# Optimization experiments

Measured on AMD Instinct MI355X. Metric: run time of the kernel, lower is better.

## Reference

```python
import jax, jax.numpy as jnp
import numpy as np

B, N, D_IMG, D_TXT, H, C = 256, 100, 1024, 768, 512, 512
NBLK = 8
EPS = 1e-5


def setup_inputs() -> dict:
    key = jax.random.key(0)
    ks = jax.random.split(key, 24)
    rn = lambda k, s, sc=0.04: jax.random.normal(k, s, jnp.float32) * sc
    return {
        "img_embedding": jax.random.normal(ks[0], (B, D_IMG), jnp.float32),
        "func_text_embedding": jax.random.normal(ks[1], (B, D_TXT), jnp.float32),
        "node_emb": jax.random.normal(ks[2], (B, N, 768), jnp.float32),
        "pos_emb": jax.random.uniform(ks[3], (B, N, 4), jnp.float32),
        # swin head
        "swinbn_g": jnp.ones((D_IMG,)), "swinbn_b": jnp.zeros((D_IMG,)),
        "swinfc_w": rn(ks[4], (H, D_IMG)), "swinfc_b": jnp.zeros((H,)),
        # text head
        "bntext_g": jnp.ones((D_TXT,)), "bntext_b": jnp.zeros((D_TXT,)),
        "fctext_w": rn(ks[5], (H, D_TXT)), "fctext_b": jnp.zeros((H,)),
        # node / bbox heads (BatchNorm1d over channel dim = max_node)
        "bngat_g": jnp.ones((N,)), "bngat_b": jnp.zeros((N,)),
        "fcgat_w": rn(ks[6], (480, 768)), "fcgat_b": jnp.zeros((480,)),
        "bnbbox_g": jnp.ones((N,)), "bnbbox_b": jnp.zeros((N,)),
        "fcbbox_w": rn(ks[7], (32, 4), 0.3), "fcbbox_b": jnp.zeros((32,)),
        # 8 stacked Rs_GCN non-local blocks (1x1 conv weights = [out,in])
        "gcn_theta_w": rn(ks[8], (NBLK, C, C)), "gcn_theta_b": jnp.zeros((NBLK, C)),
        "gcn_phi_w": rn(ks[9], (NBLK, C, C)), "gcn_phi_b": jnp.zeros((NBLK, C)),
        "gcn_g_w": rn(ks[10], (NBLK, C, C)), "gcn_g_b": jnp.zeros((NBLK, C)),
        "gcn_W_w": rn(ks[11], (NBLK, C, C)), "gcn_W_b": jnp.zeros((NBLK, C)),
        "gcn_bn_g": jnp.ones((NBLK, C)), "gcn_bn_b": jnp.zeros((NBLK, C)),
        # final classifier
        "ffbn_g": jnp.ones((3 * H,)), "ffbn_b": jnp.zeros((3 * H,)),
        "ff_w": rn(ks[12], (2, 3 * H)), "ff_b": jnp.zeros((2,)),
    }


def _bn2(x, g, b):  # BatchNorm1d on (B, C), training-mode batch stats
    m = x.mean(0)
    v = x.var(0)
    return (x - m) * jax.lax.rsqrt(v + EPS) * g + b


def _bn_ch(x, g, b):  # BatchNorm1d on (B, C, L), channel axis 1
    m = x.mean((0, 2), keepdims=True)
    v = x.var((0, 2), keepdims=True)
    return (x - m) * jax.lax.rsqrt(v + EPS) * g[None, :, None] + b[None, :, None]


def reference(img_embedding, func_text_embedding, node_emb, pos_emb,
              swinbn_g, swinbn_b, swinfc_w, swinfc_b,
              bntext_g, bntext_b, fctext_w, fctext_b,
              bngat_g, bngat_b, fcgat_w, fcgat_b,
              bnbbox_g, bnbbox_b, fcbbox_w, fcbbox_b,
              gcn_theta_w, gcn_theta_b, gcn_phi_w, gcn_phi_b,
              gcn_g_w, gcn_g_b, gcn_W_w, gcn_W_b, gcn_bn_g, gcn_bn_b,
              ffbn_g, ffbn_b, ff_w, ff_b):
    elu = jax.nn.elu
    # image branch: x = elu(swinfc(swinbn(img)))
    x = elu(_bn2(img_embedding, swinbn_g, swinbn_b) @ swinfc_w.T + swinfc_b)
    # text branch: elu(fc_text(bn_text(text)))
    ft = elu(_bn2(func_text_embedding, bntext_g, bntext_b) @ fctext_w.T + fctext_b)
    # node / bbox branches (BN over node dim, then linear over feature dim)
    h = elu(_bn_ch(node_emb, bngat_g, bngat_b) @ fcgat_w.T + fcgat_b)       # (B,N,480)
    p = elu(_bn_ch(pos_emb, bnbbox_g, bnbbox_b) @ fcbbox_w.T + fcbbox_b)    # (B,N,32)
    v = jnp.concatenate([h, p], axis=2).transpose(0, 2, 1)                  # (B,512,N)

    # 8 non-local Rs_GCN blocks
    for i in range(NBLK):
        g_v = jnp.einsum('oc,bcn->bno', gcn_g_w[i], v) + gcn_g_b[i]          # (B,N,C)
        th_v = jnp.einsum('oc,bcn->bno', gcn_theta_w[i], v) + gcn_theta_b[i]  # (B,N,C)
        ph_v = jnp.einsum('oc,bcn->bon', gcn_phi_w[i], v) + gcn_phi_b[i][:, None]  # (B,C,N)
        R = jnp.einsum('bnc,bcm->bnm', th_v, ph_v)                            # (B,N,N)
        A = jax.nn.softmax(R, axis=-1)
        y = jnp.einsum('bnm,bmc->bcn', A, g_v)                                # (B,C,N)
        Wy = jnp.einsum('oc,bcn->bon', gcn_W_w[i], y) + gcn_W_b[i][:, None]
        Wy = _bn_ch(Wy, gcn_bn_g[i], gcn_bn_b[i])
        v = Wy + v                                                            # residual

    emb = v.transpose(0, 2, 1)  # (B,N,512)
    # l2norm normalizes over dim=1 (the node dim), matching the torch code
    emb = emb / jnp.sqrt(jnp.sum(emb * emb, axis=1, keepdims=True))
    h_feature = emb.mean(axis=1)  # (B,512)

    all_feats = jnp.concatenate([x, h_feature, ft], axis=1)  # (B,1536)
    out = _bn2(all_feats, ffbn_g, ffbn_b) @ ff_w.T + ff_b    # (B,2)
    return out
```

## Files before the change

### kernel.cpp

```cpp
#include <hip/hip_runtime.h>
#include <cstddef>

#define EPS 1e-5f

constexpr int Bsz = 256;
constexpr int Nn  = 100;
constexpr int Cc  = 512;
constexpr int BN_ROWS = Bsz * Nn;

__device__ __forceinline__ void gload_lds16(const void* g, void* l) {
    __builtin_amdgcn_global_load_lds(
        (const __attribute__((address_space(1))) void*)g,
        (__attribute__((address_space(3))) void*)l, 16, 0, 0);
}

__global__ void colstats_kernel(const float* __restrict__ x, int M, int Ccols,
                                const float* __restrict__ g, const float* __restrict__ bb,
                                float* __restrict__ s, float* __restrict__ t) {
    int c = blockIdx.x;
    int r = threadIdx.x;
    float v = (r < M) ? x[(size_t)r * Ccols + c] : 0.f;
    __shared__ float ssum[256], ssq[256];
    ssum[r] = v; ssq[r] = v * v;
    __syncthreads();
    for (int off = 128; off > 0; off >>= 1) {
        if (r < off) { ssum[r] += ssum[r + off]; ssq[r] += ssq[r + off]; }
        __syncthreads();
    }
    if (r == 0) {
        float m   = ssum[0] / M;
        float var = ssq[0] / M - m * m;
        float sc  = g[c] * rsqrtf(var + EPS);
        s[c] = sc;
        t[c] = bb[c] - m * sc;
    }
}

__global__ void chstats_kernel(const float* __restrict__ x, int D,
                               const float* __restrict__ g, const float* __restrict__ bb,
                               float* __restrict__ s, float* __restrict__ t) {
    int n = blockIdx.x;
    int tid = threadIdx.x;
    int total = Bsz * D;
    float sum = 0.f, sq = 0.f;
    for (int idx = tid; idx < total; idx += blockDim.x) {
        int b = idx / D, d = idx - b * D;
        float v = x[((size_t)b * Nn + n) * D + d];
        sum += v; sq += v * v;
    }
    __shared__ float ssum[256], ssq[256];
    ssum[tid] = sum; ssq[tid] = sq;
    __syncthreads();
    for (int off = 128; off > 0; off >>= 1) {
        if (tid < off) { ssum[tid] += ssum[tid + off]; ssq[tid] += ssq[tid + off]; }
        __syncthreads();
    }
    if (tid == 0) {
        float m   = ssum[0] / total;
        float var = ssq[0] / total - m * m;
        float sc  = g[n] * rsqrtf(var + EPS);
        s[n] = sc;
        t[n] = bb[n] - m * sc;
    }
}

__global__ void chstats_part_kernel(const float* __restrict__ x, float* __restrict__ npart) {
    int n = blockIdx.x, chunk = blockIdx.y;
    int tid = threadIdx.x;
    float sum = 0.f, sq = 0.f;
    for (int i = tid; i < 3072; i += 256) {
        int rrow = i / 192;
        int q = i - rrow * 192;
        float4 f = *(const float4*)(x + ((size_t)(chunk * 16 + rrow) * Nn + n) * 768 + q * 4);
        sum += f.x + f.y + f.z + f.w;
        sq  += f.x * f.x + f.y * f.y + f.z * f.z + f.w * f.w;
    }
    __shared__ float ss[256], s2[256];
    ss[tid] = sum; s2[tid] = sq;
    __syncthreads();
    for (int off = 128; off > 0; off >>= 1) {
        if (tid < off) { ss[tid] += ss[tid + off]; s2[tid] += s2[tid + off]; }
        __syncthreads();
    }
    if (tid == 0) {
        npart[chunk * 200 + n] = ss[0];
        npart[chunk * 200 + 100 + n] = s2[0];
    }
}

__global__ void chstats_fin_kernel(const float* __restrict__ npart,
                                   const float* __restrict__ g, const float* __restrict__ bb,
                                   float* __restrict__ s, float* __restrict__ t) {
    int n = threadIdx.x;
    if (n >= 100) return;
    float sum = 0.f, sq = 0.f;
    for (int c = 0; c < 16; c++) {
        sum += npart[c * 200 + n];
        sq  += npart[c * 200 + 100 + n];
    }
    const float total = 256.f * 768.f;
    float m   = sum / total;
    float var = sq / total - m * m;
    float sc  = g[n] * rsqrtf(var + EPS);
    s[n] = sc;
    t[n] = bb[n] - m * sc;
}

__global__ void transpose_w_kernel(const float* __restrict__ w, const float* __restrict__ bias,
                                   float* __restrict__ WT, float* __restrict__ pb) {
    __shared__ float tile[32][33];
    int kb = blockIdx.x * 32, nb = blockIdx.y * 32;
    int tx = threadIdx.x & 31, ty = threadIdx.x >> 5;
#pragma unroll
    for (int i = 0; i < 4; i++) {
        int n = nb + ty + i * 8;
        tile[ty + i * 8][tx] = (n < 480) ? w[(size_t)n * 768 + kb + tx] : 0.f;
    }
    __syncthreads();
#pragma unroll
    for (int i = 0; i < 4; i++) {
        int k = kb + ty + i * 8;
        WT[(size_t)k * 512 + nb + tx] = tile[tx][ty + i * 8];
    }
    if (blockIdx.x == 0 && threadIdx.x < 32) {
        int n = nb + threadIdx.x;
        pb[n] = (n < 480) ? bias[n] : 0.f;
    }
}

template <int NORM, bool ELU, bool TB, int KS, int BYSHIFT>
__global__ __launch_bounds__(256) void gemm128_kernel(
    const float* __restrict__ A, const float* __restrict__ B0,
    const float* __restrict__ B1, int nsplit,
    const float* __restrict__ bias,
    const float* __restrict__ s, const float* __restrict__ t,
    int M, int N, int K, int lda, int ldb, int mod,
    float* __restrict__ C, int ldc, int c_off) {
    constexpr int BS = TB ? 132 : 128;
    __shared__ float As[KS * 132];
    __shared__ float Bs[KS * BS];

    int bid = blockIdx.x;
    int xcd = bid & 7;
    int l = bid >> 3;
    int by = l & ((1 << BYSHIFT) - 1);
    int bmi = l >> BYSHIFT;
    int bm_per_xcd = (int)(gridDim.x >> (3 + BYSHIFT));
    int bm = (xcd * bm_per_xcd + bmi) * 128;

    const float* B = (by < nsplit) ? B0 : B1;
    int bn = (by < nsplit ? by : by - nsplit) * 128;
    int outcol0 = c_off + by * 128;

    int tid = threadIdx.x;
    int lane = tid & 63, wave = tid >> 6;
    int tx = tid & 15, ty = tid >> 4;

    float acc[8][8] = {};

    for (int k0 = 0; k0 < K; k0 += KS) {
#pragma unroll
        for (int i = 0; i < KS / 8; i++) {
            int id = tid + i * 256;
            int row = id / (KS / 4), q = id % (KS / 4);
            int gr = bm + row;
            float4 f = *(const float4*)(A + (size_t)gr * lda + k0 + q * 4);
            if constexpr (NORM == 2) {
                int n_ = gr % mod; float sc = s[n_], sh = t[n_];
                f.x = f.x * sc + sh; f.y = f.y * sc + sh;
                f.z = f.z * sc + sh; f.w = f.w * sc + sh;
            }
            As[(q * 4 + 0) * 132 + row] = f.x;
            As[(q * 4 + 1) * 132 + row] = f.y;
            As[(q * 4 + 2) * 132 + row] = f.z;
            As[(q * 4 + 3) * 132 + row] = f.w;
        }
        if constexpr (TB) {
#pragma unroll
            for (int i = 0; i < KS / 8; i++) {
                int id = tid + i * 256;
                int row = id / (KS / 4), q = id % (KS / 4);
                int gn = bn + row;
                float4 f = make_float4(0.f, 0.f, 0.f, 0.f);
                if (gn < N) f = *(const float4*)(B + (size_t)gn * ldb + k0 + q * 4);
                Bs[(q * 4 + 0) * BS + row] = f.x;
                Bs[(q * 4 + 1) * BS + row] = f.y;
                Bs[(q * 4 + 2) * BS + row] = f.z;
                Bs[(q * 4 + 3) * BS + row] = f.w;
            }
        } else {
#pragma unroll
            for (int i = 0; i < KS / 8; i++) {
                int r = i * 8 + wave * 2 + (lane >> 5);
                gload_lds16(B + (size_t)(k0 + r) * ldb + bn + (lane & 31) * 4,
                            (char*)&Bs[r * BS]);
            }
        }
        __syncthreads();
#pragma unroll 16
        for (int kk = 0; kk < KS; kk++) {
            float4 a0 = *(const float4*)&As[kk * 132 + ty * 4];
            float4 a1 = *(const float4*)&As[kk * 132 + ty * 4 + 64];
            float4 b0 = *(const float4*)&Bs[kk * BS + tx * 4];
            float4 b1 = *(const float4*)&Bs[kk * BS + tx * 4 + 64];
            float av[8] = {a0.x, a0.y, a0.z, a0.w, a1.x, a1.y, a1.z, a1.w};
            float bv[8] = {b0.x, b0.y, b0.z, b0.w, b1.x, b1.y, b1.z, b1.w};
#pragma unroll
            for (int i = 0; i < 8; i++)
#pragma unroll
                for (int j = 0; j < 8; j++)
                    acc[i][j] = fmaf(av[i], bv[j], acc[i][j]);
        }
        __syncthreads();
    }

#pragma unroll
    for (int i = 0; i < 8; i++) {
        int r = ty * 4 + (i & 3) + ((i & 4) ? 64 : 0);
        int gr = bm + r;
        if (gr >= M) continue;
        float* crow = C + (size_t)gr * ldc + outcol0;
#pragma unroll
        for (int h = 0; h < 2; h++) {
            int cl = tx * 4 + h * 64;
            int gcol = bn + cl;
            if constexpr (TB) { if (gcol >= N) continue; }
            float4 o;
            o.x = acc[i][h * 4 + 0]; o.y = acc[i][h * 4 + 1];
            o.z = acc[i][h * 4 + 2]; o.w = acc[i][h * 4 + 3];
            if (bias) {
                o.x += bias[gcol]; o.y += bias[gcol + 1];
                o.z += bias[gcol + 2]; o.w += bias[gcol + 3];
            }
            if constexpr (ELU) {
                o.x = o.x > 0.f ? o.x : expm1f(o.x);
                o.y = o.y > 0.f ? o.y : expm1f(o.y);
                o.z = o.z > 0.f ? o.z : expm1f(o.z);
                o.w = o.w > 0.f ? o.w : expm1f(o.w);
            }
            *(float4*)(crow + cl) = o;
        }
    }
}

template <int NORM, bool ELU, bool TB>
__global__ void gemm_kernel(const float* __restrict__ A, const float* __restrict__ B,
                            const float* __restrict__ bias,
                            const float* __restrict__ s, const float* __restrict__ t,
                            int M, int N, int K, int lda, int ldb, int mod,
                            float* __restrict__ Cout, int ldc, int c_off) {
    __shared__ float As[16][65];
    __shared__ float Bs[16][65];

    int bm = blockIdx.x * 64, bn = blockIdx.y * 64;
    int tid = threadIdx.x;
    int tm = (tid >> 4) << 2;
    int tn = (tid & 15) << 2;
    float acc[4][4] = {};

    for (int k0 = 0; k0 < K; k0 += 16) {
#pragma unroll
        for (int i = 0; i < 4; i++) {
            int idx = tid + i * 256;
            {
                int rr = idx >> 4, kk = idx & 15;
                int gr = bm + rr, gk = k0 + kk;
                float av = 0.f;
                if (gr < M && gk < K) {
                    av = A[(size_t)gr * lda + gk];
                    if constexpr (NORM == 1) av = av * s[gk] + t[gk];
                    else if constexpr (NORM == 2) { int n_ = gr % mod; av = av * s[n_] + t[n_]; }
                }
                As[kk][rr] = av;
            }
            if constexpr (TB) {
                int nn = idx >> 4, kk = idx & 15;
                int gn = bn + nn, gk = k0 + kk;
                Bs[kk][nn] = (gn < N && gk < K) ? B[(size_t)gn * ldb + gk] : 0.f;
            } else {
                int kk = idx >> 6, nn = idx & 63;
                int gn = bn + nn, gk = k0 + kk;
                Bs[kk][nn] = (gn < N && gk < K) ? B[(size_t)gk * ldb + gn] : 0.f;
            }
        }
        __syncthreads();
#pragma unroll
        for (int kk = 0; kk < 16; kk++) {
            float a0[4], b0[4];
#pragma unroll
            for (int i = 0; i < 4; i++) a0[i] = As[kk][tm + i];
#pragma unroll
            for (int j = 0; j < 4; j++) b0[j] = Bs[kk][tn + j];
#pragma unroll
            for (int i = 0; i < 4; i++)
#pragma unroll
                for (int j = 0; j < 4; j++)
                    acc[i][j] = fmaf(a0[i], b0[j], acc[i][j]);
        }
        __syncthreads();
    }

#pragma unroll
    for (int i = 0; i < 4; i++) {
        int gr = bm + tm + i;
        if (gr >= M) continue;
#pragma unroll
        for (int j = 0; j < 4; j++) {
            int gn = bn + tn + j;
            if (gn >= N) continue;
            float v = acc[i][j] + (bias ? bias[gn] : 0.f);
            if constexpr (ELU) v = v > 0.f ? v : expm1f(v);
            Cout[(size_t)gr * ldc + c_off + gn] = v;
        }
    }
}

__global__ __launch_bounds__(256) void compose_kernel(
    const float* __restrict__ thw, const float* __restrict__ phw,
    const float* __restrict__ gw, const float* __restrict__ Ww,
    float* __restrict__ Mw_all, float* __restrict__ WGT_all) {
    __shared__ float As[32][33];
    __shared__ float Bs[32][68];
    int blk = blockIdx.z >> 1;
    int z = blockIdx.z & 1;
    size_t woff = (size_t)blk * Cc * Cc;
    const float* A = (z ? gw : thw) + woff;
    const float* ph = phw + woff;
    const float* W = Ww + woff;
    int bm = blockIdx.x * 32, bn = blockIdx.y * 64;
    int tid = threadIdx.x;
    int tm = (tid >> 4) * 2, tn = (tid & 15) * 4;
    float acc[2][4] = {};

    for (int k0 = 0; k0 < Cc; k0 += 32) {
#pragma unroll
        for (int i = 0; i < 4; i++) {
            int id = tid + i * 256;
            int kk = id >> 5, m = id & 31;
            As[kk][m] = A[(size_t)(k0 + kk) * Cc + bm + m];
        }
#pragma unroll
        for (int i = 0; i < 8; i++) {
            int id = tid + i * 256;
            if (z == 0) {
                int kk = id >> 6, n = id & 63;
                Bs[kk][n] = ph[(size_t)(k0 + kk) * Cc + bn + n];
            } else {
                int n = id >> 5, kk = id & 31;
                Bs[kk][n] = W[(size_t)(bn + n) * Cc + k0 + kk];
            }
        }
        __syncthreads();
#pragma unroll
        for (int kk = 0; kk < 32; kk++) {
            float a0 = As[kk][tm], a1 = As[kk][tm + 1];
            float4 b4 = *(const float4*)&Bs[kk][tn];
            acc[0][0] = fmaf(a0, b4.x, acc[0][0]);
            acc[0][1] = fmaf(a0, b4.y, acc[0][1]);
            acc[0][2] = fmaf(a0, b4.z, acc[0][2]);
            acc[0][3] = fmaf(a0, b4.w, acc[0][3]);
            acc[1][0] = fmaf(a1, b4.x, acc[1][0]);
            acc[1][1] = fmaf(a1, b4.y, acc[1][1]);
            acc[1][2] = fmaf(a1, b4.z, acc[1][2]);
            acc[1][3] = fmaf(a1, b4.w, acc[1][3]);
        }
        __syncthreads();
    }
    float* out = (z ? WGT_all : Mw_all) + woff;
    *(float4*)&out[(size_t)(bm + tm) * Cc + bn + tn] =
        make_float4(acc[0][0], acc[0][1], acc[0][2], acc[0][3]);
    *(float4*)&out[(size_t)(bm + tm + 1) * Cc + bn + tn] =
        make_float4(acc[1][0], acc[1][1], acc[1][2], acc[1][3]);
}

__global__ void qc_kernel(const float* __restrict__ phw, const float* __restrict__ thb,
                          const float* __restrict__ Ww, const float* __restrict__ gb,
                          const float* __restrict__ Wb,
                          float* __restrict__ q2a, float* __restrict__ cca) {
    int blk = blockIdx.y >> 1;
    int type = blockIdx.y & 1;
    int c = blockIdx.x;
    int l = threadIdx.x;
    float acc = 0.f;
    if (type == 0) {
        const float* phi = phw + (size_t)blk * Cc * Cc;
        const float* tb = thb + (size_t)blk * Cc;
        for (int j = l; j < Cc; j += 64) acc += phi[(size_t)j * Cc + c] * tb[j];
        for (int off = 32; off > 0; off >>= 1) acc += __shfl_xor(acc, off, 64);
        if (l == 0) q2a[blk * Cc + c] = acc;
    } else {
        const float* W = Ww + (size_t)blk * Cc * Cc;
        const float* gbb = gb + (size_t)blk * Cc;
        for (int j = l; j < Cc; j += 64) acc += W[(size_t)c * Cc + j] * gbb[j];
        for (int off = 32; off > 0; off >>= 1) acc += __shfl_xor(acc, off, 64);
        if (l == 0) cca[blk * Cc + c] = acc + Wb[(size_t)blk * Cc + c];
    }
}

__global__ void bbox_kernel(const float* __restrict__ pos, const float* __restrict__ w,
                            const float* __restrict__ bias, const float* __restrict__ s,
                            const float* __restrict__ t, float* __restrict__ V) {
    __shared__ float ws[32][4];
    int tid = threadIdx.x;
    if (tid < 128) ws[tid >> 2][tid & 3] = w[tid];
    __syncthreads();
    int r = blockIdx.x * 8 + (tid >> 5);
    int o = tid & 31;
    int n = r % Nn;
    float sc = s[n], sh = t[n];
    float p0 = pos[(size_t)r * 4 + 0] * sc + sh;
    float p1 = pos[(size_t)r * 4 + 1] * sc + sh;
    float p2 = pos[(size_t)r * 4 + 2] * sc + sh;
    float p3 = pos[(size_t)r * 4 + 3] * sc + sh;
    float acc = bias[o] + p0 * ws[o][0] + p1 * ws[o][1] + p2 * ws[o][2] + p3 * ws[o][3];
    acc = acc > 0.f ? acc : expm1f(acc);
    V[(size_t)r * Cc + 480 + o] = acc;
}

__global__ __launch_bounds__(256) void attn_fused_kernel(
    float* __restrict__ TZ, const float* __restrict__ V,
    const float* __restrict__ q2, const float* __restrict__ cc,
    float* __restrict__ part) {
    __shared__ float smem[11904];
    float* Ts = smem;
    float* Vs = smem + 1800;
    float* A_lds = smem;
    float* ct_lds = smem + 5400;
    float* Zs = smem + 5504;

    int bid = blockIdx.x;
    int xcd = bid & 7;
    int l = bid >> 3;
    int b = xcd * 32 + (l >> 1);
    int rh = l & 1;
    int row0 = b * Nn + rh * 50;
    int tid = threadIdx.x;
    int lane = tid & 63, wave = tid >> 6;
    int tx = tid & 31, ty = tid >> 5;

    {
        int r = tid >> 1, h = tid & 1;
        float cacc = 0.f;
        if (r < Nn) {
            const float4* vp = (const float4*)(V + (size_t)(b * Nn + r) * 512);
            const float4* qp = (const float4*)q2;
            for (int c4 = h; c4 < 128; c4 += 2) {
                float4 f = vp[c4], q = qp[c4];
                cacc += f.x * q.x + f.y * q.y + f.z * q.z + f.w * q.w;
            }
        }
        cacc += __shfl_xor(cacc, 1, 64);
        if (r < Nn && h == 0) ct_lds[r] = cacc;
    }

    float acc[7][4];
#pragma unroll
    for (int i = 0; i < 7; i++)
#pragma unroll
        for (int j = 0; j < 4; j++) acc[i][j] = 0.f;

    for (int kt = 0; kt < 16; kt++) {
        __syncthreads();
        for (int i = tid; i < 1200; i += 256) {
            if (i < 400) {
                int r = i >> 3, q = i & 7;
                float4 f = *(const float4*)(TZ + (size_t)(row0 + r) * 1024 + kt * 32 + q * 4);
                *(float4*)&Ts[r * 36 + q * 4] = f;
            } else {
                int ii = i - 400;
                int r = ii >> 3, q = ii & 7;
                float4 f = *(const float4*)(V + (size_t)(b * Nn + r) * 512 + kt * 32 + q * 4);
                *(float4*)&Vs[r * 36 + q * 4] = f;
            }
        }
        __syncthreads();
#pragma unroll
        for (int q = 0; q < 8; q++) {
            float4 av[7];
#pragma unroll
            for (int i = 0; i < 7; i++)
                av[i] = *(const float4*)&Ts[(ty * 7 + i) * 36 + q * 4];
            float4 bv[4];
#pragma unroll
            for (int j = 0; j < 4; j++)
                bv[j] = *(const float4*)&Vs[(tx + 32 * j) * 36 + q * 4];
#pragma unroll
            for (int kk = 0; kk < 4; kk++) {
#pragma unroll
                for (int i = 0; i < 7; i++) {
                    float a = ((const float*)&av[i])[kk];
#pragma unroll
                    for (int j = 0; j < 4; j++)
                        acc[i][j] = fmaf(a, ((const float*)&bv[j])[kk], acc[i][j]);
                }
            }
        }
    }
    __syncthreads();

    float ctv[4];
#pragma unroll
    for (int j = 0; j < 4; j++) {
        int c = tx + 32 * j;
        ctv[j] = (c < Nn) ? ct_lds[c] : 0.f;
    }
#pragma unroll
    for (int i = 0; i < 7; i++) {
        int r = ty * 7 + i;
        if (r >= 50) continue;
#pragma unroll
        for (int j = 0; j < 4; j++) {
            int c = tx + 32 * j;
            if (c < Nn) A_lds[r * 105 + c] = acc[i][j] + ctv[j];
        }
    }
    __syncthreads();
    if (tid < 50) {
        float* row = A_lds + tid * 105;
        float mx = -1e30f;
        for (int m = 0; m < Nn; m++) mx = fmaxf(mx, row[m]);
        float sm = 0.f;
        for (int m = 0; m < Nn; m++) { float e = expf(row[m] - mx); row[m] = e; sm += e; }
        float inv = 1.f / sm;
        for (int m = 0; m < Nn; m++) row[m] *= inv;
    }

    int pair = b * 2 + rh;
    for (int ch = 0; ch < 2; ch++) {
        float acc2[7][8];
#pragma unroll
        for (int i = 0; i < 7; i++)
#pragma unroll
            for (int j = 0; j < 8; j++) acc2[i][j] = 0.f;

        for (int kt = 0; kt < 4; kt++) {
            __syncthreads();
            for (int r = wave; r < 25; r += 4) {
                gload_lds16(TZ + (size_t)(b * Nn + kt * 25 + r) * 1024 + 512 + ch * 256 + lane * 4,
                            (char*)&Zs[r * 256]);
            }
            __syncthreads();
#pragma unroll 5
            for (int k2 = 0; k2 < 25; k2++) {
                int k = kt * 25 + k2;
                float av[7];
#pragma unroll
                for (int i = 0; i < 7; i++) av[i] = A_lds[(ty * 7 + i) * 105 + k];
                float zv[8];
#pragma unroll
                for (int j = 0; j < 8; j++) zv[j] = Zs[k2 * 256 + tx + 32 * j];
#pragma unroll
                for (int i = 0; i < 7; i++)
#pragma unroll
                    for (int j = 0; j < 8; j++)
                        acc2[i][j] = fmaf(av[i], zv[j], acc2[i][j]);
            }
        }

        float ccv[8];
#pragma unroll
        for (int j = 0; j < 8; j++) ccv[j] = cc[ch * 256 + tx + 32 * j];
        float psum[8], psq[8];
#pragma unroll
        for (int j = 0; j < 8; j++) { psum[j] = 0.f; psq[j] = 0.f; }
#pragma unroll
        for (int i = 0; i < 7; i++) {
            int r = ty * 7 + i;
            if (r >= 50) continue;
            float* orow = TZ + (size_t)(row0 + r) * 1024 + ch * 256;
#pragma unroll
            for (int j = 0; j < 8; j++) {
                float v = acc2[i][j] + ccv[j];
                orow[tx + 32 * j] = v;
                psum[j] += v; psq[j] += v * v;
            }
        }
        __syncthreads();
        float* sums = Zs;
#pragma unroll
        for (int j = 0; j < 8; j++) {
            int c = tx + 32 * j;
            sums[ty * 512 + c] = psum[j];
            sums[ty * 512 + 256 + c] = psq[j];
        }
        __syncthreads();
        {
            float ssv = 0.f, sqv = 0.f;
            for (int y = 0; y < 8; y++) {
                ssv += sums[y * 512 + tid];
                sqv += sums[y * 512 + 256 + tid];
            }
            part[(size_t)pair * 1024 + ch * 256 + tid] = ssv;
            part[(size_t)pair * 1024 + 512 + ch * 256 + tid] = sqv;
        }
    }
}

__global__ void wy_fin2_kernel(const float* __restrict__ part,
                               const float* __restrict__ g, const float* __restrict__ bb,
                               float* __restrict__ s, float* __restrict__ t) {
    int c = blockIdx.x;
    int l = threadIdx.x;
    float sum = 0.f, sq = 0.f;
    for (int p = l; p < 512; p += 64) {
        sum += part[(size_t)p * 1024 + c];
        sq  += part[(size_t)p * 1024 + 512 + c];
    }
    for (int off = 32; off > 0; off >>= 1) {
        sum += __shfl_xor(sum, off, 64);
        sq  += __shfl_xor(sq, off, 64);
    }
    if (l == 0) {
        float m   = sum / BN_ROWS;
        float var = sq / BN_ROWS - m * m;
        float sc  = g[c] * rsqrtf(var + EPS);
        s[c] = sc;
        t[c] = bb[c] - m * sc;
    }
}

__global__ void residual_kernel(float* __restrict__ V, const float* __restrict__ Wy, int ldw,
                                const float* __restrict__ s, const float* __restrict__ t) {
    size_t total4 = (size_t)BN_ROWS * Cc / 4;
    for (size_t i4 = (size_t)blockIdx.x * blockDim.x + threadIdx.x; i4 < total4;
         i4 += (size_t)gridDim.x * blockDim.x) {
        int row = (int)(i4 >> 7);
        int c = (int)(i4 & 127) * 4;
        float4 w = *(const float4*)(Wy + (size_t)row * ldw + c);
        float4 sv = *(const float4*)(s + c);
        float4 tv = *(const float4*)(t + c);
        float4 v = *(float4*)(V + (size_t)row * Cc + c);
        v.x += w.x * sv.x + tv.x; v.y += w.y * sv.y + tv.y;
        v.z += w.z * sv.z + tv.z; v.w += w.w * sv.w + tv.w;
        *(float4*)(V + (size_t)row * Cc + c) = v;
    }
}

__global__ void l2norm_mean_kernel(const float* __restrict__ V, float* __restrict__ ALL) {
    int b = blockIdx.x;
    int c = threadIdx.x;
    float sum = 0.f, sq = 0.f;
    const float* p = V + (size_t)b * Nn * Cc + c;
    for (int n = 0; n < Nn; n++) {
        float v = p[(size_t)n * Cc];
        sum += v; sq += v * v;
    }
    ALL[(size_t)b * 1536 + 512 + c] = sum / (Nn * sqrtf(sq));
}

__global__ void final_kernel(const float* __restrict__ ALL, const float* __restrict__ s,
                             const float* __restrict__ t, const float* __restrict__ w,
                             const float* __restrict__ bias, float* __restrict__ out) {
    int b = blockIdx.x;
    int tid = threadIdx.x;
    float p0 = 0.f, p1 = 0.f;
    for (int k = tid; k < 1536; k += 256) {
        float af = ALL[(size_t)b * 1536 + k] * s[k] + t[k];
        p0 += af * w[k];
        p1 += af * w[1536 + k];
    }
    __shared__ float s0[256], s1[256];
    s0[tid] = p0; s1[tid] = p1;
    __syncthreads();
    for (int off = 128; off > 0; off >>= 1) {
        if (tid < off) { s0[tid] += s0[tid + off]; s1[tid] += s1[tid + off]; }
        __syncthreads();
    }
    if (tid == 0) {
        out[b * 2 + 0] = s0[0] + bias[0];
        out[b * 2 + 1] = s1[0] + bias[1];
    }
}

extern "C" void kernel_launch(void* const* d_in, const int* in_sizes, int n_in,
                              void* d_out, int out_size, void* d_ws, size_t ws_size,
                              hipStream_t stream) {
    const float* img   = (const float*)d_in[0];
    const float* txt   = (const float*)d_in[1];
    const float* node  = (const float*)d_in[2];
    const float* pos   = (const float*)d_in[3];
    const float* swinbn_g = (const float*)d_in[4];
    const float* swinbn_b = (const float*)d_in[5];
    const float* swinfc_w = (const float*)d_in[6];
    const float* swinfc_b = (const float*)d_in[7];
    const float* bntext_g = (const float*)d_in[8];
    const float* bntext_b = (const float*)d_in[9];
    const float* fctext_w = (const float*)d_in[10];
    const float* fctext_b = (const float*)d_in[11];
    const float* bngat_g  = (const float*)d_in[12];
    const float* bngat_b  = (const float*)d_in[13];
    const float* fcgat_w  = (const float*)d_in[14];
    const float* fcgat_b  = (const float*)d_in[15];
    const float* bnbbox_g = (const float*)d_in[16];
    const float* bnbbox_b = (const float*)d_in[17];
    const float* fcbbox_w = (const float*)d_in[18];
    const float* fcbbox_b = (const float*)d_in[19];
    const float* gcn_theta_w = (const float*)d_in[20];
    const float* gcn_theta_b = (const float*)d_in[21];
    const float* gcn_phi_w   = (const float*)d_in[22];
    const float* gcn_phi_b   = (const float*)d_in[23];
    const float* gcn_g_w     = (const float*)d_in[24];
    const float* gcn_g_b     = (const float*)d_in[25];
    const float* gcn_W_w     = (const float*)d_in[26];
    const float* gcn_W_b     = (const float*)d_in[27];
    const float* gcn_bn_g    = (const float*)d_in[28];
    const float* gcn_bn_b    = (const float*)d_in[29];
    const float* ffbn_g = (const float*)d_in[30];
    const float* ffbn_b = (const float*)d_in[31];
    const float* ff_w   = (const float*)d_in[32];
    const float* ff_b   = (const float*)d_in[33];

    float* ws = (float*)d_ws;
    const size_t VN = (size_t)BN_ROWS * Cc;
    const size_t CC2 = (size_t)Cc * Cc;
    float* V       = ws;
    float* TZ      = V + VN;
    float* Mw_all  = TZ + VN * 2;
    float* WGT_all = Mw_all + 8 * CC2;
    float* WT      = WGT_all + 8 * CC2;
    float* ALL     = WT + 393216;
    float* part    = ALL + (size_t)Bsz * 1536;
    float* q2_all  = part + 524288;
    float* cc_all  = q2_all + 4096;
    float* st      = cc_all + 4096;
    float* s_img = st;            float* t_img = s_img + 1024;
    float* s_txt = t_img + 1024;  float* t_txt = s_txt + 768;
    float* s_nd  = t_txt + 768;   float* t_nd  = s_nd + 128;
    float* s_bb  = t_nd + 128;    float* t_bb  = s_bb + 128;
    float* s_g   = t_bb + 128;    float* t_g   = s_g + 512;
    float* s_ff  = t_g + 512;     float* t_ff  = s_ff + 1536;
    float* pb    = t_ff + 1536;

    dim3 blk(256);

    colstats_kernel<<<1024, 256, 0, stream>>>(img, 256, 1024, swinbn_g, swinbn_b, s_img, t_img);
    colstats_kernel<<<768, 256, 0, stream>>>(txt, 256, 768, bntext_g, bntext_b, s_txt, t_txt);
    chstats_part_kernel<<<dim3(100, 16, 1), 256, 0, stream>>>(node, part);
    chstats_fin_kernel<<<1, 128, 0, stream>>>(part, bngat_g, bngat_b, s_nd, t_nd);
    chstats_kernel<<<100, 256, 0, stream>>>(pos, 4, bnbbox_g, bnbbox_b, s_bb, t_bb);

    gemm_kernel<1, true, true><<<dim3(4, 8, 1), blk, 0, stream>>>(
        img, swinfc_w, swinfc_b, s_img, t_img, 256, 512, 1024, 1024, 1024, 0,
        ALL, 1536, 0);
    gemm_kernel<1, true, true><<<dim3(4, 8, 1), blk, 0, stream>>>(
        txt, fctext_w, fctext_b, s_txt, t_txt, 256, 512, 768, 768, 768, 0,
        ALL, 1536, 1024);
    transpose_w_kernel<<<dim3(24, 16, 1), blk, 0, stream>>>(fcgat_w, fcgat_b, WT, pb);
    gemm128_kernel<2, true, false, 32, 2><<<800, blk, 0, stream>>>(
        node, WT, nullptr, 4, pb, s_nd, t_nd,
        25600, 512, 768, 768, 512, 100, V, 512, 0);
    bbox_kernel<<<3200, 256, 0, stream>>>(pos, fcbbox_w, fcbbox_b, s_bb, t_bb, V);

    compose_kernel<<<dim3(16, 8, 16), blk, 0, stream>>>(
        gcn_theta_w, gcn_phi_w, gcn_g_w, gcn_W_w, Mw_all, WGT_all);
    qc_kernel<<<dim3(512, 16, 1), 64, 0, stream>>>(
        gcn_phi_w, gcn_theta_b, gcn_W_w, gcn_g_b, gcn_W_b, q2_all, cc_all);

    for (int i = 0; i < 8; i++) {
        gemm128_kernel<0, false, false, 32, 3><<<1600, blk, 0, stream>>>(
            V, Mw_all + (size_t)i * CC2, WGT_all + (size_t)i * CC2, 4,
            nullptr, nullptr, nullptr,
            25600, 1024, 512, 512, 512, 0, TZ, 1024, 0);

        attn_fused_kernel<<<512, blk, 0, stream>>>(
            TZ, V, q2_all + (size_t)i * Cc, cc_all + (size_t)i * Cc, part);

        wy_fin2_kernel<<<512, 64, 0, stream>>>(part, gcn_bn_g + (size_t)i * Cc,
                                               gcn_bn_b + (size_t)i * Cc, s_g, t_g);
        residual_kernel<<<2048, 256, 0, stream>>>(V, TZ, 1024, s_g, t_g);
    }

    l2norm_mean_kernel<<<256, 512, 0, stream>>>(V, ALL);
    colstats_kernel<<<1536, 256, 0, stream>>>(ALL, 256, 1536, ffbn_g, ffbn_b, s_ff, t_ff);
    final_kernel<<<256, 256, 0, stream>>>(ALL, s_ff, t_ff, ff_w, ff_b, (float*)d_out);
}
```

Measured before the change: 4.678 ms.

## Fuse last residual into l2norm, parallelize softmax rows, issue B loads early

The last block's residual update is folded into the l2norm/mean kernel, which avoids one full read-modify-write pass over V. The attention softmax now splits each row across four threads, using partial max and sum values kept in shared scratch, instead of one thread per row. The GEMM issues its asynchronous B-tile loads into LDS before the A-tile loads so the two transfers overlap. The residual grid size is doubled. Together these add extra syncs in the softmax and a dependency on TZ staying live until the final kernel.

```diff
diff --git a/kernel.cpp b/kernel.cpp
--- a/kernel.cpp
+++ b/kernel.cpp
@@ -159,6 +159,14 @@
     float acc[8][8] = {};
 
     for (int k0 = 0; k0 < K; k0 += KS) {
+        if constexpr (!TB) {
+#pragma unroll
+            for (int i = 0; i < KS / 8; i++) {
+                int r = i * 8 + wave * 2 + (lane >> 5);
+                gload_lds16(B + (size_t)(k0 + r) * ldb + bn + (lane & 31) * 4,
+                            (char*)&Bs[r * BS]);
+            }
+        }
 #pragma unroll
         for (int i = 0; i < KS / 8; i++) {
             int id = tid + i * 256;
@@ -187,13 +195,6 @@
                 Bs[(q * 4 + 1) * BS + row] = f.y;
                 Bs[(q * 4 + 2) * BS + row] = f.z;
                 Bs[(q * 4 + 3) * BS + row] = f.w;
-            }
-        } else {
-#pragma unroll
-            for (int i = 0; i < KS / 8; i++) {
-                int r = i * 8 + wave * 2 + (lane >> 5);
-                gload_lds16(B + (size_t)(k0 + r) * ldb + bn + (lane & 31) * 4,
-                            (char*)&Bs[r * BS]);
             }
         }
         __syncthreads();
@@ -515,14 +516,36 @@
         }
     }
     __syncthreads();
-    if (tid < 50) {
-        float* row = A_lds + tid * 105;
-        float mx = -1e30f;
-        for (int m = 0; m < Nn; m++) mx = fmaxf(mx, row[m]);
-        float sm = 0.f;
-        for (int m = 0; m < Nn; m++) { float e = expf(row[m] - mx); row[m] = e; sm += e; }
-        float inv = 1.f / sm;
-        for (int m = 0; m < Nn; m++) row[m] *= inv;
+
+    {
+        int r = tid >> 2, q = tid & 3;
+        float* pmax = Zs;
+        float* psum = Zs + 256;
+        if (r < 50) {
+            const float* row = A_lds + r * 105 + q * 25;
+            float mx = row[0];
+            for (int m = 1; m < 25; m++) mx = fmaxf(mx, row[m]);
+            pmax[r * 4 + q] = mx;
+        }
+        __syncthreads();
+        if (r < 50) {
+            float rowmax = fmaxf(fmaxf(pmax[r * 4 + 0], pmax[r * 4 + 1]),
+                                 fmaxf(pmax[r * 4 + 2], pmax[r * 4 + 3]));
+            float* row = A_lds + r * 105 + q * 25;
+            float sm = 0.f;
+            for (int m = 0; m < 25; m++) {
+                float e = expf(row[m] - rowmax);
+                row[m] = e; sm += e;
+            }
+            psum[r * 4 + q] = sm;
+        }
+        __syncthreads();
+        if (r < 50) {
+            float tot = psum[r * 4 + 0] + psum[r * 4 + 1] + psum[r * 4 + 2] + psum[r * 4 + 3];
+            float inv = 1.f / tot;
+            float* row = A_lds + r * 105 + q * 25;
+            for (int m = 0; m < 25; m++) row[m] *= inv;
+        }
     }
 
     int pair = b * 2 + rh;
@@ -636,13 +659,17 @@
     }
 }
 
-__global__ void l2norm_mean_kernel(const float* __restrict__ V, float* __restrict__ ALL) {
+__global__ void l2norm_mean_kernel(const float* __restrict__ V, const float* __restrict__ TZwy,
+                                   const float* __restrict__ s, const float* __restrict__ t,
+                                   float* __restrict__ ALL) {
     int b = blockIdx.x;
     int c = threadIdx.x;
+    float sc = s[c], sh = t[c];
     float sum = 0.f, sq = 0.f;
     const float* p = V + (size_t)b * Nn * Cc + c;
+    const float* w = TZwy + (size_t)b * Nn * 1024 + c;
     for (int n = 0; n < Nn; n++) {
-        float v = p[(size_t)n * Cc];
+        float v = p[(size_t)n * Cc] + w[(size_t)n * 1024] * sc + sh;
         sum += v; sq += v * v;
     }
     ALL[(size_t)b * 1536 + 512 + c] = sum / (Nn * sqrtf(sq));
@@ -715,7 +742,7 @@
     const size_t CC2 = (size_t)Cc * Cc;
     float* V       = ws;
     float* TZ      = V + VN;
-    float* Mw_all  = TZ + VN * 2;
+    float* Mw_all  = TZ + 2 * VN;
     float* WGT_all = Mw_all + 8 * CC2;
     float* WT      = WGT_all + 8 * CC2;
     float* ALL     = WT + 393216;
@@ -767,10 +794,12 @@
 
         wy_fin2_kernel<<<512, 64, 0, stream>>>(part, gcn_bn_g + (size_t)i * Cc,
                                                gcn_bn_b + (size_t)i * Cc, s_g, t_g);
-        residual_kernel<<<2048, 256, 0, stream>>>(V, TZ, 1024, s_g, t_g);
-    }
-
-    l2norm_mean_kernel<<<256, 512, 0, stream>>>(V, ALL);
+
+        if (i < 7)
+            residual_kernel<<<4096, 256, 0, stream>>>(V, TZ, 1024, s_g, t_g);
+    }
+
+    l2norm_mean_kernel<<<256, 512, 0, stream>>>(V, TZ, s_g, t_g, ALL);
     colstats_kernel<<<1536, 256, 0, stream>>>(ALL, 256, 1536, ffbn_g, ffbn_b, s_ff, t_ff);
     final_kernel<<<256, 256, 0, stream>>>(ALL, s_ff, t_ff, ff_w, ff_b, (float*)d_out);
 }
```

Result: no change. 4.665 ms (-0.3%).
